# Kernel optimization log

Measured on AMD Instinct MI355X. Metric: run time of the kernel, lower is better.

The kernel has to match this reference:

```python
import jax, jax.numpy as jnp
import numpy as np

B, S, H, I, G = 2, 1024, 1024, 4096, 8


def setup_inputs() -> dict:
    key = jax.random.key(0)
    k1, k2, k3, k4 = jax.random.split(key, 4)
    # kaiming-style scaled init (scale matters only for numerics, not math)
    hidden_states = jax.random.normal(k1, (B, S, H), dtype=jnp.float32)
    WG = jax.random.normal(k2, (H, G), dtype=jnp.float32) * (1.0 / np.sqrt(H))
    Wi = jax.random.normal(k3, (G, H, I), dtype=jnp.float32) * (1.0 / np.sqrt(H))
    down = jax.random.normal(k4, (I, H), dtype=jnp.float32) * (1.0 / np.sqrt(I))
    return {"hidden_states": hidden_states, "WG": WG, "Wi": Wi, "down": down, "topk": 2}


def topk_sigmoid(gate, k):
    # gate: [B,S,G] -> sigmoid gated scores masked to top-k per token
    _, idx = jax.lax.top_k(gate, k)                       # idx: [B,S,k]
    mask = (idx[..., None] == jnp.arange(gate.shape[-1])).any(axis=-2)  # [B,S,G] bool
    return jax.nn.sigmoid(gate) * mask


def reference(hidden_states, WG, Wi, down, topk):
    gate = hidden_states @ WG                             # [B,S,G]
    g = topk_sigmoid(gate, topk)                          # [B,S,G]
    # dense contraction over all groups (faithful to original einsum)
    up = jnp.einsum('bse,bsg,geo->bso', hidden_states, g, Wi)  # [B,S,I]
    act = jnp.square(jax.nn.relu(up))                     # ReLU^2
    return act @ down                                     # [B,S,H]
```

## Files before the change

kernel.cpp:

```cpp
#include <hip/hip_runtime.h>
#include <hip/hip_bf16.h>

typedef unsigned short u16;
typedef short short8_t __attribute__((ext_vector_type(8)));
typedef float f32x4 __attribute__((ext_vector_type(4)));

#define GLOBAL_AS(p) ((const __attribute__((address_space(1))) void*)(p))
#define LDS_AS(p)    ((__attribute__((address_space(3))) void*)(p))

__device__ __forceinline__ u16 f2bf(float f) {
    union { float f; unsigned int u; } x;
    x.f = f;
    unsigned int r = x.u + 0x7fffu + ((x.u >> 16) & 1u);
    return (u16)(r >> 16);
}
__device__ __forceinline__ float bf2f(u16 v) {
    union { unsigned int u; float f; } x;
    x.u = ((unsigned int)v) << 16;
    return x.f;
}

#define M_NMT   0
#define M_TE    2
#define M_TB    42
#define M_PAIR  96
#define M_RTOK  4192
#define M_RW    9312

__global__ __launch_bounds__(64) void gate_topk_kernel(
    const float* __restrict__ h, const float* __restrict__ wg, float* __restrict__ w) {
    const int t = blockIdx.x;
    const int lane = threadIdx.x;
    float acc[8];
#pragma unroll
    for (int g = 0; g < 8; ++g) acc[g] = 0.f;
    for (int e = lane; e < 1024; e += 64) {
        float hv = h[(size_t)t * 1024 + e];
        float4 r0 = *(const float4*)&wg[e * 8];
        float4 r1 = *(const float4*)&wg[e * 8 + 4];
        acc[0] += hv * r0.x; acc[1] += hv * r0.y; acc[2] += hv * r0.z; acc[3] += hv * r0.w;
        acc[4] += hv * r1.x; acc[5] += hv * r1.y; acc[6] += hv * r1.z; acc[7] += hv * r1.w;
    }
#pragma unroll
    for (int off = 32; off > 0; off >>= 1) {
#pragma unroll
        for (int g = 0; g < 8; ++g) acc[g] += __shfl_down(acc[g], off);
    }
    if (lane == 0) {
        int i1 = 0;
        for (int g = 1; g < 8; ++g) if (acc[g] > acc[i1]) i1 = g;
        int i2 = -1;
        for (int g = 0; g < 8; ++g) {
            if (g == i1) continue;
            if (i2 < 0 || acc[g] > acc[i2]) i2 = g;
        }
#pragma unroll
        for (int g = 0; g < 8; ++g) {
            float v = (g == i1 || g == i2) ? (1.f / (1.f + __expf(-acc[g]))) : 0.f;
            w[t * 8 + g] = v;
        }
    }
}

__global__ __launch_bounds__(1024) void scan_kernel(
    const float* __restrict__ w, int* __restrict__ meta) {
    __shared__ int wcnt[2][16][8];
    __shared__ int woff[2][16][8];
    __shared__ int ebase[8];
    const int tid = threadIdx.x;
    const int wv = tid >> 6;
    const int ln = tid & 63;
    const unsigned long long ltmask = (1ull << ln) - 1ull;

    for (int i = tid; i < 5120; i += 1024) meta[M_RTOK + i] = -1;

    unsigned long long msk[2][8];
#pragma unroll
    for (int p = 0; p < 2; ++p) {
        const int t = tid + p * 1024;
#pragma unroll
        for (int g = 0; g < 8; ++g) {
            const bool f = w[t * 8 + g] > 0.f;
            msk[p][g] = __ballot(f);
        }
        if (ln == 0) {
#pragma unroll
            for (int g = 0; g < 8; ++g) wcnt[p][wv][g] = __popcll(msk[p][g]);
        }
    }
    __syncthreads();
    if (tid == 0) {
        int cnt[8];
        for (int g = 0; g < 8; ++g) {
            int s = 0;
            for (int p = 0; p < 2; ++p)
                for (int v = 0; v < 16; ++v) s += wcnt[p][v][g];
            cnt[g] = s;
        }
        int base = 0, mt = 0;
        for (int e = 0; e < 8; ++e) {
            ebase[e] = base;
            int nt = (cnt[e] + 127) >> 7;
            for (int k = 0; k < nt; ++k) { meta[M_TE + mt] = e; meta[M_TB + mt] = base + k * 128; ++mt; }
            base += nt << 7;
        }
        meta[M_NMT] = mt;
        meta[1] = base;
    }
    __syncthreads();
    if (tid < 8) {
        const int g = tid;
        int run = ebase[g];
        for (int p = 0; p < 2; ++p)
            for (int v = 0; v < 16; ++v) { woff[p][v][g] = run; run += wcnt[p][v][g]; }
    }
    __syncthreads();
    float* row_w = (float*)&meta[M_RW];
#pragma unroll
    for (int p = 0; p < 2; ++p) {
        const int t = tid + p * 1024;
        int slot = 0;
#pragma unroll
        for (int g = 0; g < 8; ++g) {
            const float wval = w[t * 8 + g];
            if (wval > 0.f) {
                const int row = woff[p][wv][g] + __popcll(msk[p][g] & ltmask);
                meta[M_RTOK + row] = t;
                row_w[row] = wval;
                meta[M_PAIR + t * 2 + slot] = row;
                ++slot;
            }
        }
    }
}

__global__ __launch_bounds__(256) void gather_a_kernel(
    const float* __restrict__ h, const int* __restrict__ meta, u16* __restrict__ A) {
    const int row = blockIdx.x;
    const int tid = threadIdx.x;
    const int tok = meta[M_RTOK + row];
    u16* dst = A + (size_t)row * 1024;
    if (tok < 0) {
        uint2 z; z.x = 0u; z.y = 0u;
        ((uint2*)dst)[tid] = z;
        return;
    }
    const float wv = ((const float*)&meta[M_RW])[row];
    float4 v = ((const float4*)(h + (size_t)tok * 1024))[tid];
    u16 o[4] = { f2bf(v.x * wv), f2bf(v.y * wv), f2bf(v.z * wv), f2bf(v.w * wv) };
    ((uint2*)dst)[tid] = *(const uint2*)o;
}

__global__ __launch_bounds__(256) void gemm1_sparse_kernel(
    const u16* __restrict__ A, const float* __restrict__ Wi,
    u16* __restrict__ up, const int* __restrict__ meta) {
    const int mt = blockIdx.y;
    if (mt >= meta[M_NMT]) return;
    const int e = meta[M_TE + mt];
    const int base = meta[M_TB + mt];
    const int n0 = blockIdx.x * 128;
    const int K = 1024, N = 4096;
    const float* Bm = Wi + (size_t)e * K * N;

    __shared__ short a_tile[128 * 64];
    __shared__ short b_tile[128 * 64];
    const int tid = threadIdx.x;
    const int lane = tid & 63;
    const int wave = tid >> 6;
    const int wm = (wave >> 1) * 64;
    const int wn = (wave & 1) * 64;
    const int r = lane & 15;
    const int quad = lane >> 4;
    const int rowin = lane >> 3;
    const int achk = ((lane & 7) ^ (rowin & 7)) * 8;
    const int aldst = (lane & 7) * 8;

    const int bidx_n = tid & 127;
    const int bidx_k8 = tid >> 7;

    const f32x4 vzero = {0.f, 0.f, 0.f, 0.f};
    f32x4 acc[4][4];
#pragma unroll
    for (int i = 0; i < 4; ++i)
#pragma unroll
        for (int j = 0; j < 4; ++j) acc[i][j] = vzero;

    float bvp[2][8];
    float bvt[2][8];

#pragma unroll
    for (int cb = 0; cb < 2; ++cb) {
        const float* bp = Bm + (size_t)((bidx_k8 + cb * 2) * 8) * N + n0 + bidx_n;
#pragma unroll
        for (int kk = 0; kk < 8; ++kk) bvp[cb][kk] = bp[(size_t)kk * N];
    }

    for (int kb = 0; kb < K; kb += 64) {
#pragma unroll
        for (int it = 0; it < 4; ++it) {
            int row = wave * 8 + it * 32 + rowin;
            const u16* ga = A + (size_t)(base + row) * K + kb + achk;
            __builtin_amdgcn_global_load_lds(GLOBAL_AS(ga), LDS_AS(&a_tile[row * 64 + aldst]), 16, 0, 0);
        }
#pragma unroll
        for (int cb = 0; cb < 2; ++cb) {
            int bk8 = bidx_k8 + cb * 2;
            u16 bc[8];
#pragma unroll
            for (int kk = 0; kk < 8; ++kk) bc[kk] = f2bf(bvp[cb][kk]);
            *(short8_t*)&b_tile[bidx_n * 64 + ((bk8 ^ (bidx_n & 7)) * 8)] = *(const short8_t*)bc;
        }
#pragma unroll
        for (int cb = 0; cb < 2; ++cb) {
            const float* bp = Bm + (size_t)(kb + (bidx_k8 + (cb + 2) * 2) * 8) * N + n0 + bidx_n;
#pragma unroll
            for (int kk = 0; kk < 8; ++kk) bvt[cb][kk] = bp[(size_t)kk * N];
        }
#pragma unroll
        for (int cb = 0; cb < 2; ++cb) {
            int bk8 = bidx_k8 + (cb + 2) * 2;
            u16 bc[8];
#pragma unroll
            for (int kk = 0; kk < 8; ++kk) bc[kk] = f2bf(bvt[cb][kk]);
            *(short8_t*)&b_tile[bidx_n * 64 + ((bk8 ^ (bidx_n & 7)) * 8)] = *(const short8_t*)bc;
        }
        __syncthreads();

        if (kb + 64 < K) {
#pragma unroll
            for (int cb = 0; cb < 2; ++cb) {
                const float* bp = Bm + (size_t)(kb + 64 + (bidx_k8 + cb * 2) * 8) * N + n0 + bidx_n;
#pragma unroll
                for (int kk = 0; kk < 8; ++kk) {
                    asm volatile("global_load_dword %0, %1, off"
                                 : "=v"(bvp[cb][kk]) : "v"(bp + (size_t)kk * N));
                }
            }
        }

#pragma unroll
        for (int ks = 0; ks < 2; ++ks) {
            const int cp = ((ks * 4 + quad) ^ (r & 7)) * 8;
            short8_t af[4], bfr[4];
#pragma unroll
            for (int i = 0; i < 4; ++i)
                af[i] = *(const short8_t*)&a_tile[(wm + i * 16 + r) * 64 + cp];
#pragma unroll
            for (int j = 0; j < 4; ++j)
                bfr[j] = *(const short8_t*)&b_tile[(wn + j * 16 + r) * 64 + cp];
#pragma unroll
            for (int i = 0; i < 4; ++i)
#pragma unroll
                for (int j = 0; j < 4; ++j)
                    acc[i][j] = __builtin_amdgcn_mfma_f32_16x16x32_bf16(af[i], bfr[j], acc[i][j], 0, 0, 0);
        }
        __syncthreads();
    }
#pragma unroll
    for (int i = 0; i < 4; ++i)
#pragma unroll
        for (int j = 0; j < 4; ++j)
#pragma unroll
            for (int reg = 0; reg < 4; ++reg) {
                int cr = base + wm + i * 16 + quad * 4 + reg;
                int cc = n0 + wn + j * 16 + r;
                up[(size_t)cr * N + cc] = f2bf(acc[i][j][reg]);
            }
}

__global__ __launch_bounds__(256) void combine_kernel(
    const u16* __restrict__ up, const int* __restrict__ meta, u16* __restrict__ act) {
    const int t = blockIdx.x;
    const int tid = threadIdx.x;
    const int p0 = meta[M_PAIR + t * 2];
    const int p1 = meta[M_PAIR + t * 2 + 1];
    const u16* r0 = up + (size_t)p0 * 4096;
    const u16* r1 = up + (size_t)p1 * 4096;
    u16* dst = act + (size_t)t * 4096;
#pragma unroll
    for (int it = 0; it < 2; ++it) {
        int i = (tid + it * 256) * 8;
        short8_t a8 = *(const short8_t*)&r0[i];
        short8_t b8 = *(const short8_t*)&r1[i];
        u16 o[8];
#pragma unroll
        for (int j = 0; j < 8; ++j) {
            float s = bf2f((u16)a8[j]) + bf2f((u16)b8[j]);
            s = s > 0.f ? s * s : 0.f;
            o[j] = f2bf(s);
        }
        *(short8_t*)&dst[i] = *(const short8_t*)o;
    }
}

__global__ __launch_bounds__(256) void transpose_cvt_kernel(
    const float* __restrict__ in, u16* __restrict__ out, int R, int C) {
    __shared__ u16 tile[64][65];
    const int rt = blockIdx.y * 64;
    const int ct = blockIdx.x * 64;
    const int tid = threadIdx.x;
#pragma unroll
    for (int it = 0; it < 2; ++it) {
        int r = (tid >> 3) + it * 32;
        int c8 = (tid & 7) * 8;
        const float* ip = &in[(size_t)(rt + r) * C + ct + c8];
        float4 v0 = *(const float4*)ip;
        float4 v1 = *(const float4*)(ip + 4);
        tile[c8 + 0][r] = f2bf(v0.x); tile[c8 + 1][r] = f2bf(v0.y);
        tile[c8 + 2][r] = f2bf(v0.z); tile[c8 + 3][r] = f2bf(v0.w);
        tile[c8 + 4][r] = f2bf(v1.x); tile[c8 + 5][r] = f2bf(v1.y);
        tile[c8 + 6][r] = f2bf(v1.z); tile[c8 + 7][r] = f2bf(v1.w);
    }
    __syncthreads();
#pragma unroll
    for (int it = 0; it < 2; ++it) {
        int c = (tid >> 3) + it * 32;
        int r8 = (tid & 7) * 8;
        u16 tmp[8];
#pragma unroll
        for (int j = 0; j < 8; ++j) tmp[j] = tile[c][r8 + j];
        *(uint4*)&out[(size_t)(ct + c) * R + rt + r8] = *(const uint4*)tmp;
    }
}

template <int BM, int WROWS, int WCOLS>
__global__ __launch_bounds__(256) void gemm_tn_kernel(
    const u16* __restrict__ X, const u16* __restrict__ Y, float* __restrict__ Pout,
    int M, int N, int K) {
    constexpr int WM = BM / WROWS;
    constexpr int WN = 128 / WCOLS;
    constexpr int FI = WM / 16;
    constexpr int FJ = WN / 16;
    __shared__ short a_tile[2][BM * 64];
    __shared__ short b_tile[2][128 * 64];
    const int tid = threadIdx.x;
    const int lane = tid & 63;
    const int wave = tid >> 6;

    const int Nt = gridDim.x, Mt = gridDim.y;
    const int lid = blockIdx.y * Nt + blockIdx.x;
    const int xcd = lid & 7;
    const int p = lid >> 3;
    const int mpx = Mt >> 3;
    const int m_tile = xcd * mpx + (p % mpx);
    const int n_tile = p / mpx;
    const int m0 = m_tile * BM;
    const int n0 = n_tile * 128;
    const int kchunk = K >> 2;
    const int kb0 = blockIdx.z * kchunk;

    const int wm = (wave / WCOLS) * WM;
    const int wn = (wave % WCOLS) * WN;
    const int rowin = lane >> 3;
    const int achk = ((lane & 7) ^ (rowin & 7)) * 8;
    const int aldst = (lane & 7) * 8;
    const int r = lane & 15;
    const int quad = lane >> 4;

    const f32x4 vzero = {0.f, 0.f, 0.f, 0.f};
    f32x4 acc[FI][FJ];
#pragma unroll
    for (int i = 0; i < FI; ++i)
#pragma unroll
        for (int j = 0; j < FJ; ++j) acc[i][j] = vzero;

#define G2_STAGE(kb_, buf)                                                            \
    {                                                                                 \
        const int kbc = (kb_);                                                        \
        _Pragma("unroll")                                                             \
        for (int it = 0; it < BM / 32; ++it) {                                        \
            int row = wave * 8 + it * 32 + rowin;                                     \
            const u16* ga = X + (size_t)(m0 + row) * K + kbc + achk;                  \
            __builtin_amdgcn_global_load_lds(GLOBAL_AS(ga),                           \
                LDS_AS(&a_tile[buf][row * 64 + aldst]), 16, 0, 0);                    \
        }                                                                             \
        _Pragma("unroll")                                                             \
        for (int it = 0; it < 4; ++it) {                                              \
            int row = wave * 8 + it * 32 + rowin;                                     \
            const u16* gb = Y + (size_t)(n0 + row) * K + kbc + achk;                  \
            __builtin_amdgcn_global_load_lds(GLOBAL_AS(gb),                           \
                LDS_AS(&b_tile[buf][row * 64 + aldst]), 16, 0, 0);                    \
        }                                                                             \
    }

#define G2_COMPUTE(buf)                                                               \
    {                                                                                 \
        _Pragma("unroll")                                                             \
        for (int ks = 0; ks < 2; ++ks) {                                              \
            const int cp = ((ks * 4 + quad) ^ (r & 7)) * 8;                           \
            short8_t af[FI], bfr[FJ];                                                 \
            _Pragma("unroll")                                                         \
            for (int i = 0; i < FI; ++i)                                              \
                af[i] = *(const short8_t*)&a_tile[buf][(wm + i * 16 + r) * 64 + cp];  \
            _Pragma("unroll")                                                         \
            for (int j = 0; j < FJ; ++j)                                              \
                bfr[j] = *(const short8_t*)&b_tile[buf][(wn + j * 16 + r) * 64 + cp]; \
            _Pragma("unroll")                                                         \
            for (int i = 0; i < FI; ++i)                                              \
                _Pragma("unroll")                                                     \
                for (int j = 0; j < FJ; ++j)                                          \
                    acc[i][j] = __builtin_amdgcn_mfma_f32_16x16x32_bf16(              \
                        af[i], bfr[j], acc[i][j], 0, 0, 0);                           \
        }                                                                             \
    }

    const int nk = kchunk >> 6;
    G2_STAGE(kb0, 0);
    __syncthreads();
    for (int t = 0; t < nk - 1; ++t) {
        const int nxt = (t + 1) & 1;
        G2_STAGE(kb0 + (t + 1) * 64, nxt);
        G2_COMPUTE(t & 1);
        __syncthreads();
    }
    G2_COMPUTE((nk - 1) & 1);

#undef G2_STAGE
#undef G2_COMPUTE

    float* Co = Pout + (size_t)blockIdx.z * M * N;
#pragma unroll
    for (int i = 0; i < FI; ++i)
#pragma unroll
        for (int j = 0; j < FJ; ++j)
#pragma unroll
            for (int reg = 0; reg < 4; ++reg) {
                int cr = m0 + wm + i * 16 + quad * 4 + reg;
                int cc = n0 + wn + j * 16 + r;
                Co[(size_t)cr * N + cc] = acc[i][j][reg];
            }
}

__global__ __launch_bounds__(256) void reduce4_kernel(
    const float* __restrict__ P, float* __restrict__ out) {
    const size_t S = (size_t)2048 * 1024;
    size_t i = ((size_t)blockIdx.x * 256 + threadIdx.x) * 4;
    float4 a = *(const float4*)&P[i];
    float4 b = *(const float4*)&P[S + i];
    float4 c = *(const float4*)&P[2 * S + i];
    float4 d = *(const float4*)&P[3 * S + i];
    float4 o;
    o.x = (a.x + b.x) + (c.x + d.x);
    o.y = (a.y + b.y) + (c.y + d.y);
    o.z = (a.z + b.z) + (c.z + d.z);
    o.w = (a.w + b.w) + (c.w + d.w);
    *(float4*)&out[i] = o;
}

extern "C" void kernel_launch(void* const* d_in, const int* in_sizes, int n_in,
                              void* d_out, int out_size, void* d_ws, size_t ws_size,
                              hipStream_t stream) {
    const float* h    = (const float*)d_in[0];
    const float* WG   = (const float*)d_in[1];
    const float* Wi   = (const float*)d_in[2];
    const float* down = (const float*)d_in[3];
    float* out = (float*)d_out;

    const int T = 2048, H = 1024, I = 4096;

    char* ws = (char*)d_ws;
    float* w_gate = (float*)(ws);
    int*   meta   = (int*)(ws + 65536);
    u16*   Arow   = (u16*)(ws + 131072);
    u16*   up     = (u16*)(ws + 131072 + 10485760);
    u16*   act    = (u16*)(ws + 131072 + 10485760 + 83886080);
    u16*   downT  = (u16*)(ws + 131072 + 10485760 + 83886080 + 16777216);
    float* part   = (float*)(ws + 131072 + 10485760);

    gate_topk_kernel<<<T, 64, 0, stream>>>(h, WG, w_gate);
    scan_kernel<<<1, 1024, 0, stream>>>(w_gate, meta);
    gather_a_kernel<<<5120, 256, 0, stream>>>(h, meta, Arow);

    gemm1_sparse_kernel<<<dim3(32, 40), 256, 0, stream>>>(Arow, Wi, up, meta);

    combine_kernel<<<T, 256, 0, stream>>>(up, meta, act);

    transpose_cvt_kernel<<<dim3(H / 64, I / 64), 256, 0, stream>>>(down, downT, I, H);
    gemm_tn_kernel<128, 2, 2><<<dim3(H / 128, T / 128, 4), 256, 0, stream>>>(
        act, downT, part, T, H, I);
    reduce4_kernel<<<(T * H) / 1024, 256, 0, stream>>>(part, out);
}
```

Measured before the change: 328.3 us.

## Fuse expert-combine and ReLU² into down-projection GEMM A-tile loads; bf16 partials

Removes the separate combine kernel: the down-projection GEMM now gathers each token's two expert up rows, sums them, applies ReLU² and writes the swizzled A tile into LDS directly, so the act buffer round-trip and one launch disappear. The split-K partials are stored as bf16 instead of fp32, halving partial write and reduce traffic. In exchange the A-tile path becomes synchronous register loads plus ALU work inside the main loop instead of async global_load_lds, which may limit overlap. Rounding the partial sums to bf16 adds precision error.

Measured after the change: 340.0 us. 1.04x slower.

```diff
diff --git a/kernel.cpp b/kernel.cpp
--- a/kernel.cpp
+++ b/kernel.cpp
@@ -268,31 +268,6 @@
             }
 }
 
-__global__ __launch_bounds__(256) void combine_kernel(
-    const u16* __restrict__ up, const int* __restrict__ meta, u16* __restrict__ act) {
-    const int t = blockIdx.x;
-    const int tid = threadIdx.x;
-    const int p0 = meta[M_PAIR + t * 2];
-    const int p1 = meta[M_PAIR + t * 2 + 1];
-    const u16* r0 = up + (size_t)p0 * 4096;
-    const u16* r1 = up + (size_t)p1 * 4096;
-    u16* dst = act + (size_t)t * 4096;
-#pragma unroll
-    for (int it = 0; it < 2; ++it) {
-        int i = (tid + it * 256) * 8;
-        short8_t a8 = *(const short8_t*)&r0[i];
-        short8_t b8 = *(const short8_t*)&r1[i];
-        u16 o[8];
-#pragma unroll
-        for (int j = 0; j < 8; ++j) {
-            float s = bf2f((u16)a8[j]) + bf2f((u16)b8[j]);
-            s = s > 0.f ? s * s : 0.f;
-            o[j] = f2bf(s);
-        }
-        *(short8_t*)&dst[i] = *(const short8_t*)o;
-    }
-}
-
 __global__ __launch_bounds__(256) void transpose_cvt_kernel(
     const float* __restrict__ in, u16* __restrict__ out, int R, int C) {
     __shared__ u16 tile[64][65];
@@ -323,128 +298,144 @@
     }
 }
 
-template <int BM, int WROWS, int WCOLS>
-__global__ __launch_bounds__(256) void gemm_tn_kernel(
-    const u16* __restrict__ X, const u16* __restrict__ Y, float* __restrict__ Pout,
-    int M, int N, int K) {
-    constexpr int WM = BM / WROWS;
-    constexpr int WN = 128 / WCOLS;
-    constexpr int FI = WM / 16;
-    constexpr int FJ = WN / 16;
-    __shared__ short a_tile[2][BM * 64];
+__global__ __launch_bounds__(256) void gemm2_fused_kernel(
+    const u16* __restrict__ up, const int* __restrict__ meta,
+    const u16* __restrict__ Y, u16* __restrict__ Pout) {
+    const int M = 2048, N = 1024;
+    const int lid = blockIdx.y * 8 + blockIdx.x;
+    const int xcd = lid & 7;
+    const int p = lid >> 3;
+    const int m_tile = xcd * 2 + (p & 1);
+    const int n_tile = p >> 1;
+    const int m0 = m_tile * 128;
+    const int n0 = n_tile * 128;
+    const int kb0 = blockIdx.z * 1024;
+
+    __shared__ short a_tile[2][128 * 64];
     __shared__ short b_tile[2][128 * 64];
     const int tid = threadIdx.x;
     const int lane = tid & 63;
     const int wave = tid >> 6;
-
-    const int Nt = gridDim.x, Mt = gridDim.y;
-    const int lid = blockIdx.y * Nt + blockIdx.x;
-    const int xcd = lid & 7;
-    const int p = lid >> 3;
-    const int mpx = Mt >> 3;
-    const int m_tile = xcd * mpx + (p % mpx);
-    const int n_tile = p / mpx;
-    const int m0 = m_tile * BM;
-    const int n0 = n_tile * 128;
-    const int kchunk = K >> 2;
-    const int kb0 = blockIdx.z * kchunk;
-
-    const int wm = (wave / WCOLS) * WM;
-    const int wn = (wave % WCOLS) * WN;
+    const int wm = (wave >> 1) * 64;
+    const int wn = (wave & 1) * 64;
+    const int r = lane & 15;
+    const int quad = lane >> 4;
     const int rowin = lane >> 3;
     const int achk = ((lane & 7) ^ (rowin & 7)) * 8;
     const int aldst = (lane & 7) * 8;
-    const int r = lane & 15;
-    const int quad = lane >> 4;
+
+    const int arow = tid & 127;
+    const int ahalf = tid >> 7;
+    const int tok = m0 + arow;
+    const int q0 = meta[M_PAIR + tok * 2];
+    const int q1 = meta[M_PAIR + tok * 2 + 1];
+    const u16* u0 = up + (size_t)q0 * 4096 + kb0;
+    const u16* u1 = up + (size_t)q1 * 4096 + kb0;
+    const int aswz = arow & 7;
 
     const f32x4 vzero = {0.f, 0.f, 0.f, 0.f};
-    f32x4 acc[FI][FJ];
-#pragma unroll
-    for (int i = 0; i < FI; ++i)
-#pragma unroll
-        for (int j = 0; j < FJ; ++j) acc[i][j] = vzero;
-
-#define G2_STAGE(kb_, buf)                                                            \
+    f32x4 acc[4][4];
+#pragma unroll
+    for (int i = 0; i < 4; ++i)
+#pragma unroll
+        for (int j = 0; j < 4; ++j) acc[i][j] = vzero;
+
+#define GF_STAGEA(kb_, buf)                                                           \
     {                                                                                 \
         const int kbc = (kb_);                                                        \
         _Pragma("unroll")                                                             \
-        for (int it = 0; it < BM / 32; ++it) {                                        \
-            int row = wave * 8 + it * 32 + rowin;                                     \
-            const u16* ga = X + (size_t)(m0 + row) * K + kbc + achk;                  \
-            __builtin_amdgcn_global_load_lds(GLOBAL_AS(ga),                           \
-                LDS_AS(&a_tile[buf][row * 64 + aldst]), 16, 0, 0);                    \
+        for (int c4 = 0; c4 < 4; ++c4) {                                              \
+            const int kc = ahalf * 4 + c4;                                            \
+            short8_t a8 = *(const short8_t*)&u0[kbc + kc * 8];                        \
+            short8_t b8 = *(const short8_t*)&u1[kbc + kc * 8];                        \
+            u16 o[8];                                                                 \
+            _Pragma("unroll")                                                         \
+            for (int j = 0; j < 8; ++j) {                                             \
+                float s = bf2f((u16)a8[j]) + bf2f((u16)b8[j]);                        \
+                s = s > 0.f ? s * s : 0.f;                                            \
+                o[j] = f2bf(s);                                                       \
+            }                                                                         \
+            *(short8_t*)&a_tile[buf][arow * 64 + ((kc ^ aswz) * 8)] =                  \
+                *(const short8_t*)o;                                                  \
         }                                                                             \
+    }
+
+#define GF_STAGEB(kb_, buf)                                                           \
+    {                                                                                 \
+        const int kbc = (kb_);                                                        \
         _Pragma("unroll")                                                             \
         for (int it = 0; it < 4; ++it) {                                              \
             int row = wave * 8 + it * 32 + rowin;                                     \
-            const u16* gb = Y + (size_t)(n0 + row) * K + kbc + achk;                  \
+            const u16* gb = Y + (size_t)(n0 + row) * 4096 + kb0 + kbc + achk;         \
             __builtin_amdgcn_global_load_lds(GLOBAL_AS(gb),                           \
                 LDS_AS(&b_tile[buf][row * 64 + aldst]), 16, 0, 0);                    \
         }                                                                             \
     }
 
-#define G2_COMPUTE(buf)                                                               \
+#define GF_COMPUTE(buf)                                                               \
     {                                                                                 \
         _Pragma("unroll")                                                             \
         for (int ks = 0; ks < 2; ++ks) {                                              \
             const int cp = ((ks * 4 + quad) ^ (r & 7)) * 8;                           \
-            short8_t af[FI], bfr[FJ];                                                 \
+            short8_t af[4], bfr[4];                                                   \
             _Pragma("unroll")                                                         \
-            for (int i = 0; i < FI; ++i)                                              \
+            for (int i = 0; i < 4; ++i)                                               \
                 af[i] = *(const short8_t*)&a_tile[buf][(wm + i * 16 + r) * 64 + cp];  \
             _Pragma("unroll")                                                         \
-            for (int j = 0; j < FJ; ++j)                                              \
+            for (int j = 0; j < 4; ++j)                                               \
                 bfr[j] = *(const short8_t*)&b_tile[buf][(wn + j * 16 + r) * 64 + cp]; \
             _Pragma("unroll")                                                         \
-            for (int i = 0; i < FI; ++i)                                              \
+            for (int i = 0; i < 4; ++i)                                               \
                 _Pragma("unroll")                                                     \
-                for (int j = 0; j < FJ; ++j)                                          \
+                for (int j = 0; j < 4; ++j)                                           \
                     acc[i][j] = __builtin_amdgcn_mfma_f32_16x16x32_bf16(              \
                         af[i], bfr[j], acc[i][j], 0, 0, 0);                           \
         }                                                                             \
     }
 
-    const int nk = kchunk >> 6;
-    G2_STAGE(kb0, 0);
+    GF_STAGEB(0, 0);
+    GF_STAGEA(0, 0);
     __syncthreads();
-    for (int t = 0; t < nk - 1; ++t) {
+    for (int t = 0; t < 15; ++t) {
         const int nxt = (t + 1) & 1;
-        G2_STAGE(kb0 + (t + 1) * 64, nxt);
-        G2_COMPUTE(t & 1);
+        GF_STAGEB((t + 1) * 64, nxt);
+        GF_STAGEA((t + 1) * 64, nxt);
+        GF_COMPUTE(t & 1);
         __syncthreads();
     }
-    G2_COMPUTE((nk - 1) & 1);
-
-#undef G2_STAGE
-#undef G2_COMPUTE
-
-    float* Co = Pout + (size_t)blockIdx.z * M * N;
-#pragma unroll
-    for (int i = 0; i < FI; ++i)
-#pragma unroll
-        for (int j = 0; j < FJ; ++j)
+    GF_COMPUTE(1);
+
+#undef GF_STAGEA
+#undef GF_STAGEB
+#undef GF_COMPUTE
+
+    u16* Co = Pout + (size_t)blockIdx.z * M * N;
+#pragma unroll
+    for (int i = 0; i < 4; ++i)
+#pragma unroll
+        for (int j = 0; j < 4; ++j)
 #pragma unroll
             for (int reg = 0; reg < 4; ++reg) {
                 int cr = m0 + wm + i * 16 + quad * 4 + reg;
                 int cc = n0 + wn + j * 16 + r;
-                Co[(size_t)cr * N + cc] = acc[i][j][reg];
+                Co[(size_t)cr * N + cc] = f2bf(acc[i][j][reg]);
             }
 }
 
 __global__ __launch_bounds__(256) void reduce4_kernel(
-    const float* __restrict__ P, float* __restrict__ out) {
+    const u16* __restrict__ P, float* __restrict__ out) {
     const size_t S = (size_t)2048 * 1024;
-    size_t i = ((size_t)blockIdx.x * 256 + threadIdx.x) * 4;
-    float4 a = *(const float4*)&P[i];
-    float4 b = *(const float4*)&P[S + i];
-    float4 c = *(const float4*)&P[2 * S + i];
-    float4 d = *(const float4*)&P[3 * S + i];
-    float4 o;
-    o.x = (a.x + b.x) + (c.x + d.x);
-    o.y = (a.y + b.y) + (c.y + d.y);
-    o.z = (a.z + b.z) + (c.z + d.z);
-    o.w = (a.w + b.w) + (c.w + d.w);
-    *(float4*)&out[i] = o;
+    size_t i = ((size_t)blockIdx.x * 256 + threadIdx.x) * 8;
+    short8_t a = *(const short8_t*)&P[i];
+    short8_t b = *(const short8_t*)&P[S + i];
+    short8_t c = *(const short8_t*)&P[2 * S + i];
+    short8_t d = *(const short8_t*)&P[3 * S + i];
+    float o[8];
+#pragma unroll
+    for (int j = 0; j < 8; ++j)
+        o[j] = (bf2f((u16)a[j]) + bf2f((u16)b[j])) + (bf2f((u16)c[j]) + bf2f((u16)d[j]));
+    *(float4*)&out[i] = *(const float4*)&o[0];
+    *(float4*)&out[i + 4] = *(const float4*)&o[4];
 }
 
 extern "C" void kernel_launch(void* const* d_in, const int* in_sizes, int n_in,
@@ -463,9 +454,8 @@
     int*   meta   = (int*)(ws + 65536);
     u16*   Arow   = (u16*)(ws + 131072);
     u16*   up     = (u16*)(ws + 131072 + 10485760);
-    u16*   act    = (u16*)(ws + 131072 + 10485760 + 83886080);
+    u16*   part   = (u16*)(ws + 131072 + 10485760 + 83886080);
     u16*   downT  = (u16*)(ws + 131072 + 10485760 + 83886080 + 16777216);
-    float* part   = (float*)(ws + 131072 + 10485760);
 
     gate_topk_kernel<<<T, 64, 0, stream>>>(h, WG, w_gate);
     scan_kernel<<<1, 1024, 0, stream>>>(w_gate, meta);
@@ -473,10 +463,7 @@
 
     gemm1_sparse_kernel<<<dim3(32, 40), 256, 0, stream>>>(Arow, Wi, up, meta);
 
-    combine_kernel<<<T, 256, 0, stream>>>(up, meta, act);
-
     transpose_cvt_kernel<<<dim3(H / 64, I / 64), 256, 0, stream>>>(down, downT, I, H);
-    gemm_tn_kernel<128, 2, 2><<<dim3(H / 128, T / 128, 4), 256, 0, stream>>>(
-        act, downT, part, T, H, I);
-    reduce4_kernel<<<(T * H) / 1024, 256, 0, stream>>>(part, out);
-}
+    gemm2_fused_kernel<<<dim3(8, 16, 4), 256, 0, stream>>>(up, meta, downT, part);
+    reduce4_kernel<<<(T * H) / 2048, 256, 0, stream>>>(part, out);
+}
```
